# Kernel optimization log

Hardware: AMD Instinct MI355X
Metric: run time of the kernel (lower is better)

The kernel has to match this reference:

```python
import jax, jax.numpy as jnp
import numpy as np


def setup_inputs() -> dict:
    key = jax.random.key(0)
    kx, kw = jax.random.split(key)
    x = jax.random.normal(kx, (8192, 4096), dtype=jnp.float32)
    # weights initialized ~ N(0, 0.1) as in RandomNormal(stddev=0.1)
    w = jax.random.normal(kw, (4096, 4096), dtype=jnp.float32) * 0.1
    return {"x": x, "w": w}


def reference(x, w):
    # BinaryDense: sign-binarize both activations and weights, then matmul.
    x_bin = jnp.sign(x)  # [N, d_in], values in {-1, 0, +1}
    w_bin = jnp.sign(w)  # [d_in, units]
    return jnp.matmul(x_bin, w_bin)  # [N, units]
```

## Files before the change

### kernel.cpp

```cpp
#include <hip/hip_runtime.h>


#define M_DIM 8192
#define K_DIM 4096
#define N_DIM 4096
#define KB2   (K_DIM / 2)
#define BKB   128
#define NKT   (KB2 / BKB)
#define TILEB (256 * BKB)
#define BUFB  (2 * TILEB)

typedef int   v4i  __attribute__((ext_vector_type(4)));
typedef int   v8i  __attribute__((ext_vector_type(8)));
typedef float v16f __attribute__((ext_vector_type(16)));

__device__ __forceinline__ unsigned int nib4(float x) {
    return x > 0.0f ? 0x2u : (x < 0.0f ? 0xAu : 0x0u);
}

__global__ __launch_bounds__(256) void pack_both(const float* __restrict__ x,
                                                 unsigned short* __restrict__ xq,
                                                 const float* __restrict__ w,
                                                 unsigned char* __restrict__ wT) {
    if (blockIdx.x < 32768u) {
        size_t t = (size_t)blockIdx.x * 256 + threadIdx.x;
        float4 f = ((const float4*)x)[t];
        unsigned int v = nib4(f.x) | (nib4(f.y) << 4) | (nib4(f.z) << 8) | (nib4(f.w) << 12);
        xq[t] = (unsigned short)v;
        return;
    }
    __shared__ unsigned char sT[64][132];
    const unsigned id = blockIdx.x - 32768u;
    const int t  = threadIdx.x;
    const int n0 = (int)(id & 31) * 128;
    const int kb = (int)(id >> 5);
    const int k0 = kb * 64;

    const int cq = t & 31;
    const int r0 = t >> 5;
#pragma unroll
    for (int p = 0; p < 8; ++p) {
        int r = r0 + 8 * p;
        float4 f = *(const float4*)(w + (size_t)(k0 + r) * N_DIM + n0 + cq * 4);
        uchar4 c;
        c.x = (unsigned char)nib4(f.x);
        c.y = (unsigned char)nib4(f.y);
        c.z = (unsigned char)nib4(f.z);
        c.w = (unsigned char)nib4(f.w);
        *(uchar4*)(&sT[r][cq * 4]) = c;
    }
    __syncthreads();

    const int n  = t >> 1;
    const int kq = t & 1;
    union { unsigned char b[16]; int4 v; } u;
#pragma unroll
    for (int j = 0; j < 16; ++j) {
        unsigned lo = sT[kq * 32 + 2 * j][n];
        unsigned hi = sT[kq * 32 + 2 * j + 1][n];
        u.b[j] = (unsigned char)(lo | (hi << 4));
    }
    *(int4*)(wT + (size_t)(n0 + n) * KB2 + (size_t)kb * 32 + kq * 16) = u.v;
}

__device__ __forceinline__ v8i widen(v4i x) {
    v8i r;
    r[0] = x[0]; r[1] = x[1]; r[2] = x[2]; r[3] = x[3];
    r[4] = 0; r[5] = 0; r[6] = 0; r[7] = 0;
    return r;
}

__device__ __forceinline__ void gload16(const unsigned char* g, unsigned char* l) {
    __builtin_amdgcn_global_load_lds(
        (__attribute__((address_space(1))) void*)(void*)g,
        (__attribute__((address_space(3))) void*)l, 16, 0, 0);
}

__global__ __launch_bounds__(512, 2) void bgemm_fp4(const unsigned char* __restrict__ A,
                                                    const unsigned char* __restrict__ B,
                                                    float* __restrict__ C) {
    __shared__ __align__(16) unsigned char lds[2 * BUFB];

    const int tid  = threadIdx.x;
    const int lane = tid & 63;
    const int wave = tid >> 6;
    const int wm   = wave >> 2;
    const int wn   = wave & 3;
    const int l31  = lane & 31;
    const int lhi  = lane >> 5;

    const int m0 = blockIdx.y * 256;
    const int n0 = blockIdx.x * 256;

    v16f acc[4][2] = {};

    const unsigned char* gA[4];
    const unsigned char* gB[4];
    int dstOff[4];
#pragma unroll
    for (int i = 0; i < 4; ++i) {
        int g   = i * 512 + tid;
        int row = g >> 3;
        int kc  = (g & 7) ^ (row & 7);
        gA[i] = A + (size_t)(m0 + row) * KB2 + kc * 16;
        gB[i] = B + (size_t)(n0 + row) * KB2 + kc * 16;
        dstOff[i] = g * 16;
    }

    int offA[4][4], offB[4][2];
#pragma unroll
    for (int ks = 0; ks < 4; ++ks) {
#pragma unroll
        for (int tm = 0; tm < 4; ++tm) {
            int r  = wm * 128 + tm * 32 + l31;
            int kc = (2 * ks + lhi) ^ (r & 7);
            offA[ks][tm] = r * BKB + kc * 16;
        }
#pragma unroll
        for (int tn = 0; tn < 2; ++tn) {
            int r  = wn * 64 + tn * 32 + l31;
            int kc = (2 * ks + lhi) ^ (r & 7);
            offB[ks][tn] = r * BKB + kc * 16;
        }
    }

    auto stage = [&](int kt, int b) {
        unsigned char* s = lds + b * BUFB;
        const size_t ko = (size_t)kt * BKB;
#pragma unroll
        for (int i = 0; i < 4; ++i) {
            gload16(gA[i] + ko, s + dstOff[i]);
            gload16(gB[i] + ko, s + TILEB + dstOff[i]);
        }
    };

    auto compute = [&](int b) {
        const unsigned char* sA = lds + b * BUFB;
        const unsigned char* sB = sA + TILEB;
#pragma unroll
        for (int ks = 0; ks < 4; ++ks) {
            v4i a4[4], b4[2];
#pragma unroll
            for (int tm = 0; tm < 4; ++tm) a4[tm] = *(const v4i*)(sA + offA[ks][tm]);
#pragma unroll
            for (int tn = 0; tn < 2; ++tn) b4[tn] = *(const v4i*)(sB + offB[ks][tn]);
#pragma unroll
            for (int tm = 0; tm < 4; ++tm)
#pragma unroll
                for (int tn = 0; tn < 2; ++tn)
                    acc[tm][tn] = __builtin_amdgcn_mfma_scale_f32_32x32x64_f8f6f4(
                        widen(a4[tm]), widen(b4[tn]), acc[tm][tn],
                        4, 4,
                        0, 0x7F7F7F7F,
                        0, 0x7F7F7F7F);
        }
    };

    stage(0, 0);
    for (int kt = 0; kt < NKT; ++kt) {
        __syncthreads();
        if (kt + 1 < NKT) stage(kt + 1, (kt + 1) & 1);
        compute(kt & 1);
    }

#pragma unroll
    for (int tm = 0; tm < 4; ++tm) {
#pragma unroll
        for (int tn = 0; tn < 2; ++tn) {
            const int col  = n0 + wn * 64 + tn * 32 + l31;
            const int rowb = m0 + wm * 128 + tm * 32 + 4 * lhi;
#pragma unroll
            for (int r = 0; r < 16; ++r) {
                int row = rowb + (r & 3) + 8 * (r >> 2);
                __builtin_nontemporal_store(acc[tm][tn][r], &C[(size_t)row * N_DIM + col]);
            }
        }
    }
}

extern "C" void kernel_launch(void* const* d_in, const int* in_sizes, int n_in,
                              void* d_out, int out_size, void* d_ws, size_t ws_size,
                              hipStream_t stream) {
    const float* x = (const float*)d_in[0];
    const float* w = (const float*)d_in[1];
    float* out = (float*)d_out;

    unsigned char* xq = (unsigned char*)d_ws;
    unsigned char* wq = xq + (size_t)M_DIM * KB2;

    pack_both<<<dim3(32768 + 2048), dim3(256), 0, stream>>>(
        x, (unsigned short*)xq, w, wq);
    bgemm_fp4<<<dim3(N_DIM / 256, M_DIM / 256), dim3(512), 0, stream>>>(xq, wq, out);
}
```

Before: 321.6 us.

## Use four-slot half-K pipeline with partial vmcnt waits and MFMA priority

Splits each K tile into smaller 64-byte halves held in a four-slot LDS ring, keeping three loads in flight. It waits with partial vmcnt counts instead of a full __syncthreads drain, so global-to-LDS copies overlap compute more deeply. It also changes the LDS layout so two rows pack into each 128-byte line with an XOR swizzle, and raises wave priority around the MFMA bursts. The cost is more barriers per unit of work and hand-coded waitcnt values that must exactly match the number of outstanding loads.

```diff
diff --git a/kernel.cpp b/kernel.cpp
--- a/kernel.cpp
+++ b/kernel.cpp
@@ -5,10 +5,10 @@
 #define K_DIM 4096
 #define N_DIM 4096
 #define KB2   (K_DIM / 2)
-#define BKB   128
-#define NKT   (KB2 / BKB)
-#define TILEB (256 * BKB)
-#define BUFB  (2 * TILEB)
+#define HALFB 64
+#define NH    (KB2 / HALFB)
+#define HTILE (256 * HALFB)
+#define SLOTB (2 * HTILE)
 
 typedef int   v4i  __attribute__((ext_vector_type(4)));
 typedef int   v8i  __attribute__((ext_vector_type(8)));
@@ -79,7 +79,7 @@
 __global__ __launch_bounds__(512, 2) void bgemm_fp4(const unsigned char* __restrict__ A,
                                                     const unsigned char* __restrict__ B,
                                                     float* __restrict__ C) {
-    __shared__ __align__(16) unsigned char lds[2 * BUFB];
+    __shared__ __align__(16) unsigned char lds[4 * SLOTB];
 
     const int tid  = threadIdx.x;
     const int lane = tid & 63;
@@ -94,56 +94,62 @@
 
     v16f acc[4][2] = {};
 
-    const unsigned char* gA[4];
-    const unsigned char* gB[4];
-    int dstOff[4];
-#pragma unroll
-    for (int i = 0; i < 4; ++i) {
+    const unsigned char* gAsrc[2];
+    const unsigned char* gBsrc[2];
+    int dstOff[2];
+#pragma unroll
+    for (int i = 0; i < 2; ++i) {
         int g   = i * 512 + tid;
-        int row = g >> 3;
-        int kc  = (g & 7) ^ (row & 7);
-        gA[i] = A + (size_t)(m0 + row) * KB2 + kc * 16;
-        gB[i] = B + (size_t)(n0 + row) * KB2 + kc * 16;
+        int q   = g >> 3;
+        int t   = (g & 7) ^ (q & 7);
+        int row = 2 * q + (t >> 2);
+        int kc  = t & 3;
+        gAsrc[i] = A + (size_t)(m0 + row) * KB2 + kc * 16;
+        gBsrc[i] = B + (size_t)(n0 + row) * KB2 + kc * 16;
         dstOff[i] = g * 16;
     }
 
-    int offA[4][4], offB[4][2];
-#pragma unroll
-    for (int ks = 0; ks < 4; ++ks) {
+    int offA[2][4], offB[2][2];
+#pragma unroll
+    for (int ks = 0; ks < 2; ++ks) {
+        const int kc = 2 * ks + lhi;
 #pragma unroll
         for (int tm = 0; tm < 4; ++tm) {
-            int r  = wm * 128 + tm * 32 + l31;
-            int kc = (2 * ks + lhi) ^ (r & 7);
-            offA[ks][tm] = r * BKB + kc * 16;
+            int r    = wm * 128 + tm * 32 + l31;
+            int q    = r >> 1;
+            int slot = (((r & 1) << 2) | kc) ^ (q & 7);
+            offA[ks][tm] = q * 128 + slot * 16;
         }
 #pragma unroll
         for (int tn = 0; tn < 2; ++tn) {
-            int r  = wn * 64 + tn * 32 + l31;
-            int kc = (2 * ks + lhi) ^ (r & 7);
-            offB[ks][tn] = r * BKB + kc * 16;
-        }
-    }
-
-    auto stage = [&](int kt, int b) {
-        unsigned char* s = lds + b * BUFB;
-        const size_t ko = (size_t)kt * BKB;
-#pragma unroll
-        for (int i = 0; i < 4; ++i) {
-            gload16(gA[i] + ko, s + dstOff[i]);
-            gload16(gB[i] + ko, s + TILEB + dstOff[i]);
+            int r    = wn * 64 + tn * 32 + l31;
+            int q    = r >> 1;
+            int slot = (((r & 1) << 2) | kc) ^ (q & 7);
+            offB[ks][tn] = q * 128 + slot * 16;
+        }
+    }
+
+    auto stage = [&](int h) {
+        unsigned char* s = lds + (h & 3) * SLOTB;
+        const size_t ko = (size_t)h * HALFB;
+#pragma unroll
+        for (int i = 0; i < 2; ++i) {
+            gload16(gAsrc[i] + ko, s + dstOff[i]);
+            gload16(gBsrc[i] + ko, s + HTILE + dstOff[i]);
         }
     };
 
-    auto compute = [&](int b) {
-        const unsigned char* sA = lds + b * BUFB;
-        const unsigned char* sB = sA + TILEB;
-#pragma unroll
-        for (int ks = 0; ks < 4; ++ks) {
+    auto compute = [&](int h) {
+        const unsigned char* sA = lds + (h & 3) * SLOTB;
+        const unsigned char* sB = sA + HTILE;
+#pragma unroll
+        for (int ks = 0; ks < 2; ++ks) {
             v4i a4[4], b4[2];
 #pragma unroll
             for (int tm = 0; tm < 4; ++tm) a4[tm] = *(const v4i*)(sA + offA[ks][tm]);
 #pragma unroll
             for (int tn = 0; tn < 2; ++tn) b4[tn] = *(const v4i*)(sB + offB[ks][tn]);
+            __builtin_amdgcn_s_setprio(1);
 #pragma unroll
             for (int tm = 0; tm < 4; ++tm)
 #pragma unroll
@@ -153,15 +159,26 @@
                         4, 4,
                         0, 0x7F7F7F7F,
                         0, 0x7F7F7F7F);
+            __builtin_amdgcn_s_setprio(0);
         }
     };
 
-    stage(0, 0);
-    for (int kt = 0; kt < NKT; ++kt) {
-        __syncthreads();
-        if (kt + 1 < NKT) stage(kt + 1, (kt + 1) & 1);
-        compute(kt & 1);
-    }
+    stage(0); stage(1); stage(2);
+    for (int h = 0; h < NH - 3; ++h) {
+        asm volatile("s_waitcnt vmcnt(8)" ::: "memory");
+        __builtin_amdgcn_s_barrier();
+        stage(h + 3);
+        compute(h);
+    }
+    asm volatile("s_waitcnt vmcnt(8)" ::: "memory");
+    __builtin_amdgcn_s_barrier();
+    compute(NH - 3);
+    asm volatile("s_waitcnt vmcnt(4)" ::: "memory");
+    __builtin_amdgcn_s_barrier();
+    compute(NH - 2);
+    asm volatile("s_waitcnt vmcnt(0)" ::: "memory");
+    __builtin_amdgcn_s_barrier();
+    compute(NH - 1);
 
 #pragma unroll
     for (int tm = 0; tm < 4; ++tm) {
```

Result: no change. 324.6 us (+0.9%).
